# Optimization experiments

Hardware: AMD Instinct MI355X
Metric: run time of the kernel (lower is better)

Reference implementation:

```python
import jax, jax.numpy as jnp
import numpy as np

D = 1024
H = 16
HD = D // H
FF = 4096
B, S = 2, 2048


def _ln(x, g, b, eps):
    mu = jnp.mean(x, axis=-1, keepdims=True)
    var = jnp.mean(jnp.square(x - mu), axis=-1, keepdims=True)
    return (x - mu) * jax.lax.rsqrt(var + eps) * g + b


def setup_inputs() -> dict:
    key = jax.random.key(0)
    ks = jax.random.split(key, 12)
    s = 0.02
    return {
        "x": jax.random.normal(ks[0], (B, S, D), jnp.float32),
        "attention_mask": jnp.ones((B, 1, 1, S), jnp.int32),
        "wq": jax.random.normal(ks[1], (D, D), jnp.float32) * s,
        "bq": jnp.zeros((D,), jnp.float32),
        "wk": jax.random.normal(ks[2], (D, D), jnp.float32) * s,
        "bk": jnp.zeros((D,), jnp.float32),
        "wv": jax.random.normal(ks[3], (D, D), jnp.float32) * s,
        "bv": jnp.zeros((D,), jnp.float32),
        "wo": jax.random.normal(ks[4], (D, D), jnp.float32) * s,
        "bo": jnp.zeros((D,), jnp.float32),
        "ln1_g": jnp.ones((D,), jnp.float32),
        "ln1_b": jnp.zeros((D,), jnp.float32),
        "w1": jax.random.normal(ks[5], (D, FF), jnp.float32) * s,
        "b1": jnp.zeros((FF,), jnp.float32),
        "w2": jax.random.normal(ks[6], (FF, D), jnp.float32) * s,
        "b2": jnp.zeros((D,), jnp.float32),
        "lnf_g": jnp.ones((D,), jnp.float32),
        "lnf_b": jnp.zeros((D,), jnp.float32),
        "ln2_g": jnp.ones((D,), jnp.float32),
        "ln2_b": jnp.zeros((D,), jnp.float32),
    }


def reference(x, attention_mask, wq, bq, wk, bk, wv, bv, wo, bo,
              ln1_g, ln1_b, w1, b1, w2, b2, lnf_g, lnf_b, ln2_g, ln2_b):
    b, s, d = x.shape
    # --- naive multi-head self-attention ---
    q = (x @ wq + bq).reshape(b, s, H, HD).transpose(0, 2, 1, 3)  # [b,h,s,hd]
    k = (x @ wk + bk).reshape(b, s, H, HD).transpose(0, 2, 1, 3)
    v = (x @ wv + bv).reshape(b, s, H, HD).transpose(0, 2, 1, 3)
    scores = jnp.einsum('bhqd,bhkd->bhqk', q, k) / jnp.sqrt(jnp.float32(HD))
    scores = jnp.where(attention_mask == 0, jnp.float32(-1e9), scores)
    attn = jax.nn.softmax(scores, axis=-1)
    ctx = jnp.einsum('bhqk,bhkd->bhqd', attn, v)
    ctx = ctx.transpose(0, 2, 1, 3).reshape(b, s, d)
    attn_out = ctx @ wo + bo
    # residual + LayerNorm (eps=1e-5, torch default)
    x1 = _ln(x + attn_out, ln1_g, ln1_b, 1e-5)
    # --- BERT-style FFN with internal residual LN (eps=1e-12) ---
    h = jax.nn.gelu(x1 @ w1 + b1, approximate=False)
    ff = _ln(h @ w2 + b2 + x1, lnf_g, lnf_b, 1e-12)
    # --- outer residual + LayerNorm (eps=1e-5) ---
    return _ln(x1 + ff, ln2_g, ln2_b, 1e-5)
```

## Files before the change

### kernel.cpp

```cpp
#include <hip/hip_runtime.h>

#define DMODEL 1024
#define NHEAD  16
#define HDIM   64
#define FFDIM  4096
#define BATCH  2
#define SEQ    2048
#define MTOK   (BATCH*SEQ)

typedef __bf16 bf16;
typedef __bf16 bf16x8 __attribute__((ext_vector_type(8)));
typedef __bf16 bf16x4 __attribute__((ext_vector_type(4)));
typedef float  floatx4 __attribute__((ext_vector_type(4)));
typedef unsigned int u32;
typedef unsigned int u32x4 __attribute__((ext_vector_type(4)));

__device__ __forceinline__ int get_flag(const void* ln1g) {
  return (((const u32*)ln1g)[0] == 0x3F800000u) ? 0 : 1;
}
__device__ __forceinline__ float ld_ext(const void* p, size_t i, int flag) {
  return flag ? (float)((const bf16*)p)[i] : ((const float*)p)[i];
}

__device__ __forceinline__ void gload16(const bf16* g, bf16* lds_uniform) {
  __builtin_amdgcn_global_load_lds(
      (const __attribute__((address_space(1))) u32*)g,
      (__attribute__((address_space(3))) u32*)lds_uniform, 16, 0, 0);
}

__device__ __forceinline__ float gelu_f(float v) {
  float e = __expf(-1.702f * v);
  return __fdividef(v, 1.0f + e);
}

__global__ __launch_bounds__(256) void prep(
    const void* wq, const void* wk, const void* wv, const void* wo,
    const void* w1, const void* w2, const void* x, const int* mask,
    bf16* WTqkv, bf16* WToT, bf16* WT1, bf16* WT2, bf16* xC,
    u32* mwAll, bf16* m01All, const void* ln1g)
{
  int flag = get_flag(ln1g);
  int bid = blockIdx.x;
  if (bid >= 16384) {
    int b = bid - 16384;
    int base = b * SEQ + threadIdx.x * 8;
    #pragma unroll
    for (int j = 0; j < 8; j++)
      m01All[base + j] = (bf16)(mask[base + j] ? 1.0f : 0.0f);
    #pragma unroll
    for (int t = 0; t < 4; t++) {
      int k0 = threadIdx.x * 8 + 2 * t;
      u32 mw = (mask[b * SEQ + k0] ? 0x0000FFFFu : 0u) |
               (mask[b * SEQ + k0 + 1] ? 0xFFFF0000u : 0u);
      mwAll[b * (SEQ / 2) + threadIdx.x * 4 + t] = mw;
    }
    return;
  }
  if (bid >= 12288) {
    size_t base = (size_t)(bid - 12288) * 1024;
    int i = threadIdx.x * 4;
    #pragma unroll
    for (int j = 0; j < 4; j++) xC[base + i + j] = (bf16)ld_ext(x, base + i + j, flag);
    return;
  }
  __shared__ bf16 tile[32][33];
  const void* in; bf16* out; int K, N, t;
  if      (bid < 1024)  { in = wq; out = WTqkv;                 K = 1024; N = 1024; t = bid; }
  else if (bid < 2048)  { in = wk; out = WTqkv + 1024 * 1024;   K = 1024; N = 1024; t = bid - 1024; }
  else if (bid < 3072)  { in = wv; out = WTqkv + 2 * 1024 * 1024; K = 1024; N = 1024; t = bid - 2048; }
  else if (bid < 4096)  { in = wo; out = WToT;                  K = 1024; N = 1024; t = bid - 3072; }
  else if (bid < 8192)  { in = w1; out = WT1;                   K = 1024; N = 4096; t = bid - 4096; }
  else                  { in = w2; out = WT2;                   K = 4096; N = 1024; t = bid - 8192; }
  int shift = (N == 4096) ? 7 : 5;
  int k0 = (t >> shift) * 32, n0 = (t & ((1 << shift) - 1)) * 32;
  int tx = threadIdx.x & 31, ty = threadIdx.x >> 5;
  #pragma unroll
  for (int i = ty; i < 32; i += 8)
    tile[i][tx] = (bf16)ld_ext(in, (size_t)(k0 + i) * N + n0 + tx, flag);
  __syncthreads();
  #pragma unroll
  for (int i = ty; i < 32; i += 8)
    out[(size_t)(n0 + i) * K + k0 + tx] = tile[tx][i];
}

__global__ __launch_bounds__(256) void gemm128(
    const bf16* __restrict__ A, const bf16* __restrict__ BT,
    const void* __restrict__ bias0, const void* __restrict__ bias1,
    const void* __restrict__ bias2,
    bf16* __restrict__ out0, bf16* __restrict__ out1, bf16* __restrict__ out2,
    int N, int K, int ksub, int mode, const void* __restrict__ ln1g)
{
  __shared__ __align__(16) char smem[34816];
  bf16* As = (bf16*)smem;
  bf16* Bs = (bf16*)(smem + 16384);
  int flag = get_flag(ln1g);

  int tid = threadIdx.x, lane = tid & 63, w = tid >> 6;
  int wm = w & 1, wn = w >> 1;
  int m0 = blockIdx.x * 128, n0 = blockIdx.y * 128;
  int kstart = blockIdx.z * ksub;
  int r15 = lane & 15, kg = lane >> 4;

  floatx4 acc[4][4];
  #pragma unroll
  for (int mt = 0; mt < 4; mt++)
    #pragma unroll
    for (int nt = 0; nt < 4; nt++) acc[mt][nt] = (floatx4){0.f, 0.f, 0.f, 0.f};

  int srow8 = lane >> 3;
  int skc = (lane & 7) ^ (srow8 & 7);
  const bf16* Ap = A  + (size_t)(m0 + w * 32 + srow8) * K + kstart + skc * 8;
  const bf16* Bp = BT + (size_t)(n0 + w * 32 + srow8) * K + kstart + skc * 8;
  const size_t jstr = (size_t)8 * K;

  for (int it = ksub >> 6; it > 0; it--) {
    #pragma unroll
    for (int j = 0; j < 4; j++) {
      gload16(Ap + j * jstr, As + (size_t)(w * 256 + j * 64) * 8);
      gload16(Bp + j * jstr, Bs + (size_t)(w * 256 + j * 64) * 8);
    }
    Ap += 64; Bp += 64;
    __syncthreads();

    #pragma unroll
    for (int kk = 0; kk < 2; kk++) {
      bf16x8 af[4], bfr[4];
      #pragma unroll
      for (int mt = 0; mt < 4; mt++) {
        int row = wm * 64 + mt * 16 + r15;
        int slot = (kk * 4 + kg) ^ (r15 & 7);
        af[mt] = *(const bf16x8*)&As[(row * 8 + slot) * 8];
      }
      #pragma unroll
      for (int nt = 0; nt < 4; nt++) {
        int row = wn * 64 + nt * 16 + r15;
        int slot = (kk * 4 + kg) ^ (r15 & 7);
        bfr[nt] = *(const bf16x8*)&Bs[(row * 8 + slot) * 8];
      }
      #pragma unroll
      for (int mt = 0; mt < 4; mt++)
        #pragma unroll
        for (int nt = 0; nt < 4; nt++)
          acc[mt][nt] = __builtin_amdgcn_mfma_f32_16x16x32_bf16(af[mt], bfr[nt], acc[mt][nt], 0, 0, 0);
    }
    __syncthreads();
  }

  bf16* scr = (bf16*)(smem + 8704 * w);
  int gcb = n0 + wn * 64;
  int which = (mode == 1) ? (gcb >> 10) : 0;
  int rowg0 = m0 + wm * 64;

  #pragma unroll
  for (int nt = 0; nt < 4; nt++) {
    int lcol = nt * 16 + r15;
    int gcol = gcb + lcol;
    int bidx = (mode == 1) ? (gcol & 1023) : gcol;
    const void* bp = (mode == 1) ? ((which == 0) ? bias0 : (which == 1) ? bias1 : bias2) : bias0;
    float bv = (blockIdx.z == 0) ? ld_ext(bp, bidx, flag) : 0.f;
    #pragma unroll
    for (int mt = 0; mt < 4; mt++) {
      #pragma unroll
      for (int r = 0; r < 4; r++) {
        int lrow = mt * 16 + kg * 4 + r;
        float val = acc[mt][nt][r] + bv;
        if (mode == 2) val = gelu_f(val);
        if (mode == 1 && which == 0) val *= 0.125f;
        if (mode == 1 && which == 2) scr[lcol * 68 + lrow] = (bf16)val;
        else                         scr[lrow * 68 + lcol] = (bf16)val;
      }
    }
  }
  __syncthreads();

  bf16* outp = out0 + (size_t)blockIdx.z * MTOK * N;
  #pragma unroll
  for (int it = 0; it < 8; it++) {
    int c = it * 64 + lane;
    int rr = c >> 3, part = c & 7;
    bf16x8 vdat = *(const bf16x8*)&scr[rr * 68 + part * 8];
    bf16* dst;
    if (mode == 1) {
      if (which == 2) {
        int h = (gcb - 2048) >> 6, hd = rr;
        int b = rowg0 >> 11, s0 = rowg0 & 2047;
        dst = out2 + ((size_t)(b * NHEAD + h) * HDIM + hd) * SEQ + s0 + part * 8;
      } else {
        int rowg = rowg0 + rr;
        int b = rowg >> 11, s = rowg & 2047;
        int h = (gcb & 1023) >> 6;
        bf16* o = (which == 0) ? out0 : out1;
        dst = o + ((size_t)(b * NHEAD + h) * SEQ + s) * HDIM + part * 8;
      }
    } else {
      dst = outp + (size_t)(rowg0 + rr) * N + gcb + part * 8;
    }
    *(bf16x8*)dst = vdat;
  }
}

__global__ __launch_bounds__(256) void attn_mfma(
    const bf16* __restrict__ q, const bf16* __restrict__ k,
    const bf16* __restrict__ vt, const u32* __restrict__ mwAll,
    const bf16* __restrict__ m01All, bf16* __restrict__ ctx)
{
  __shared__ __align__(16) bf16 Ks[4096];
  __shared__ __align__(16) bf16 Vts[4096];
  __shared__ __align__(16) bf16 Ps[4][2048];

  int tid = threadIdx.x, lane = tid & 63, w = tid >> 6;
  int r15 = lane & 15, kg = lane >> 4;
  int x7 = r15 & 7;
  int bh = blockIdx.x >> 4;
  int qt = blockIdx.x & 15;
  int b = bh >> 4, h = bh & 15;
  int q0 = qt * 128 + w * 32;

  bf16x8 qf[2][2];
  #pragma unroll
  for (int mt = 0; mt < 2; mt++)
    #pragma unroll
    for (int kt2 = 0; kt2 < 2; kt2++)
      qf[mt][kt2] = *(const bf16x8*)(q + ((size_t)bh * SEQ + q0 + mt * 16 + r15) * HDIM + kt2 * 32 + kg * 8);

  floatx4 O[2][4];
  floatx4 lacc[2];
  #pragma unroll
  for (int mt = 0; mt < 2; mt++) {
    lacc[mt] = (floatx4){0.f, 0.f, 0.f, 0.f};
    #pragma unroll
    for (int dt = 0; dt < 4; dt++) O[mt][dt] = (floatx4){0.f, 0.f, 0.f, 0.f};
  }

  int slo = kg ^ x7, shi = (kg + 4) ^ x7;
  const bf16* pap[2][2];
  #pragma unroll
  for (int mt = 0; mt < 2; mt++) {
    pap[mt][0] = &Ps[w][((mt * 16 + r15) * 8 + slo) * 8];
    pap[mt][1] = &Ps[w][((mt * 16 + r15) * 8 + shi) * 8];
  }

  for (int kt = 0; kt < SEQ; kt += 64) {
    #pragma unroll
    for (int j = 0; j < 2; j++) {
      int c = w * 128 + j * 64 + lane;
      int row = c >> 3, cc = c & 7;
      gload16(k + ((size_t)bh * SEQ + kt + row) * HDIM + (cc ^ (row & 7)) * 8,
              Ks + (size_t)(w * 128 + j * 64) * 8);
    }
    #pragma unroll
    for (int j = 0; j < 2; j++) {
      int c = tid + j * 256;
      int row = c >> 3, cc = c & 7;
      u32x4 vv = *(const u32x4*)(vt + ((size_t)bh * HDIM + row) * SEQ + kt + cc * 8);
      u32x4 mw = *(const u32x4*)&mwAll[(size_t)b * (SEQ / 2) + (kt + cc * 8) / 2];
      vv &= mw;
      *(u32x4*)&Vts[(row * 8 + (cc ^ (row & 7))) * 8] = vv;
    }
    __syncthreads();

    floatx4 S[2][4];
    #pragma unroll
    for (int mt = 0; mt < 2; mt++)
      #pragma unroll
      for (int nt = 0; nt < 4; nt++) S[mt][nt] = (floatx4){0.f, 0.f, 0.f, 0.f};
    #pragma unroll
    for (int nt = 0; nt < 4; nt++) {
      int rb = (nt * 16 + r15) * 8;
      bf16x8 kf0 = *(const bf16x8*)&Ks[(rb + slo) * 8];
      bf16x8 kf1 = *(const bf16x8*)&Ks[(rb + shi) * 8];
      #pragma unroll
      for (int mt = 0; mt < 2; mt++) {
        S[mt][nt] = __builtin_amdgcn_mfma_f32_16x16x32_bf16(kf0, qf[mt][0], S[mt][nt], 0, 0, 0);
        S[mt][nt] = __builtin_amdgcn_mfma_f32_16x16x32_bf16(kf1, qf[mt][1], S[mt][nt], 0, 0, 0);
      }
    }

    #pragma unroll
    for (int mt = 0; mt < 2; mt++)
      #pragma unroll
      for (int nt = 0; nt < 4; nt++) {
        bf16x4 pk;
        #pragma unroll
        for (int r = 0; r < 4; r++) pk[r] = (bf16)__expf(S[mt][nt][r]);
        int c2 = 2 * nt + (kg >> 1);
        *(bf16x4*)&Ps[w][((mt * 16 + r15) * 8 + (c2 ^ x7)) * 8 + (kg & 1) * 4] = pk;
      }

    bf16x8 pa[2][2];
    #pragma unroll
    for (int mt = 0; mt < 2; mt++) {
      pa[mt][0] = *(const bf16x8*)pap[mt][0];
      pa[mt][1] = *(const bf16x8*)pap[mt][1];
    }
    bf16x8 m01f0 = *(const bf16x8*)&m01All[(size_t)b * SEQ + kt + kg * 8];
    bf16x8 m01f1 = *(const bf16x8*)&m01All[(size_t)b * SEQ + kt + 32 + kg * 8];
    #pragma unroll
    for (int dt = 0; dt < 4; dt++) {
      int rb = (dt * 16 + r15) * 8;
      bf16x8 vf0 = *(const bf16x8*)&Vts[(rb + slo) * 8];
      bf16x8 vf1 = *(const bf16x8*)&Vts[(rb + shi) * 8];
      #pragma unroll
      for (int mt = 0; mt < 2; mt++) {
        O[mt][dt] = __builtin_amdgcn_mfma_f32_16x16x32_bf16(pa[mt][0], vf0, O[mt][dt], 0, 0, 0);
        O[mt][dt] = __builtin_amdgcn_mfma_f32_16x16x32_bf16(pa[mt][1], vf1, O[mt][dt], 0, 0, 0);
      }
    }
    #pragma unroll
    for (int mt = 0; mt < 2; mt++) {
      lacc[mt] = __builtin_amdgcn_mfma_f32_16x16x32_bf16(pa[mt][0], m01f0, lacc[mt], 0, 0, 0);
      lacc[mt] = __builtin_amdgcn_mfma_f32_16x16x32_bf16(pa[mt][1], m01f1, lacc[mt], 0, 0, 0);
    }
    __syncthreads();
  }

  #pragma unroll
  for (int mt = 0; mt < 2; mt++) {
    float inv[4];
    #pragma unroll
    for (int r = 0; r < 4; r++) inv[r] = 1.f / lacc[mt][r];
    #pragma unroll
    for (int dt = 0; dt < 4; dt++)
      #pragma unroll
      for (int r = 0; r < 4; r++) {
        int srow = q0 + mt * 16 + kg * 4 + r;
        int col = h * 64 + dt * 16 + r15;
        ctx[((size_t)b * SEQ + srow) * DMODEL + col] = (bf16)(O[mt][dt][r] * inv[r]);
      }
  }
}

__global__ __launch_bounds__(256) void ln_kernel(
    const bf16* ba, const bf16* bb, const bf16* bc,
    const void* g, const void* be, float eps, bf16* outb, const void* ln1g)
{
  __shared__ float red1[4], red2[4];
  int flag = get_flag(ln1g);
  size_t base = (size_t)blockIdx.x * DMODEL;
  float v[4];
  #pragma unroll
  for (int i = 0; i < 4; i++) {
    int idx = threadIdx.x + i * 256;
    float s = (float)ba[base + idx] + (float)bb[base + idx] + (float)bc[base + idx];
    v[i] = s;
  }
  float sum = v[0] + v[1] + v[2] + v[3];
  #pragma unroll
  for (int o = 32; o > 0; o >>= 1) sum += __shfl_xor(sum, o);
  if ((threadIdx.x & 63) == 0) red1[threadIdx.x >> 6] = sum;
  __syncthreads();
  float mean = (red1[0] + red1[1] + red1[2] + red1[3]) * (1.f / DMODEL);
  float sq = 0.f;
  #pragma unroll
  for (int i = 0; i < 4; i++) { v[i] -= mean; sq += v[i] * v[i]; }
  #pragma unroll
  for (int o = 32; o > 0; o >>= 1) sq += __shfl_xor(sq, o);
  if ((threadIdx.x & 63) == 0) red2[threadIdx.x >> 6] = sq;
  __syncthreads();
  float rstd = rsqrtf((red2[0] + red2[1] + red2[2] + red2[3]) * (1.f / DMODEL) + eps);
  #pragma unroll
  for (int i = 0; i < 4; i++) {
    int idx = threadIdx.x + i * 256;
    outb[base + idx] = (bf16)(v[i] * rstd * ld_ext(g, idx, flag) + ld_ext(be, idx, flag));
  }
}

__global__ __launch_bounds__(256) void ln_double(
    const bf16* p0, const bf16* p1, const bf16* x1,
    const void* gf, const void* bf, const void* g2, const void* b2,
    void* out_ext, const void* ln1g)
{
  __shared__ float red1[4], red2[4];
  int flag = get_flag(ln1g);
  size_t base = (size_t)blockIdx.x * DMODEL;
  float xv[4], v[4];
  #pragma unroll
  for (int i = 0; i < 4; i++) {
    int idx = threadIdx.x + i * 256;
    xv[i] = (float)x1[base + idx];
    v[i] = xv[i] + (float)p0[base + idx] + (float)p1[base + idx];
  }
  float sum = v[0] + v[1] + v[2] + v[3];
  #pragma unroll
  for (int o = 32; o > 0; o >>= 1) sum += __shfl_xor(sum, o);
  if ((threadIdx.x & 63) == 0) red1[threadIdx.x >> 6] = sum;
  __syncthreads();
  float mean = (red1[0] + red1[1] + red1[2] + red1[3]) * (1.f / DMODEL);
  float sq = 0.f;
  #pragma unroll
  for (int i = 0; i < 4; i++) { v[i] -= mean; sq += v[i] * v[i]; }
  #pragma unroll
  for (int o = 32; o > 0; o >>= 1) sq += __shfl_xor(sq, o);
  if ((threadIdx.x & 63) == 0) red2[threadIdx.x >> 6] = sq;
  __syncthreads();
  float rstd = rsqrtf((red2[0] + red2[1] + red2[2] + red2[3]) * (1.f / DMODEL) + 1e-12f);
  #pragma unroll
  for (int i = 0; i < 4; i++) {
    int idx = threadIdx.x + i * 256;
    float ff = v[i] * rstd * ld_ext(gf, idx, flag) + ld_ext(bf, idx, flag);
    v[i] = xv[i] + (float)(bf16)ff;
  }
  __syncthreads();
  sum = v[0] + v[1] + v[2] + v[3];
  #pragma unroll
  for (int o = 32; o > 0; o >>= 1) sum += __shfl_xor(sum, o);
  if ((threadIdx.x & 63) == 0) red1[threadIdx.x >> 6] = sum;
  __syncthreads();
  mean = (red1[0] + red1[1] + red1[2] + red1[3]) * (1.f / DMODEL);
  sq = 0.f;
  #pragma unroll
  for (int i = 0; i < 4; i++) { v[i] -= mean; sq += v[i] * v[i]; }
  #pragma unroll
  for (int o = 32; o > 0; o >>= 1) sq += __shfl_xor(sq, o);
  if ((threadIdx.x & 63) == 0) red2[threadIdx.x >> 6] = sq;
  __syncthreads();
  rstd = rsqrtf((red2[0] + red2[1] + red2[2] + red2[3]) * (1.f / DMODEL) + 1e-5f);
  #pragma unroll
  for (int i = 0; i < 4; i++) {
    int idx = threadIdx.x + i * 256;
    float y = v[i] * rstd * ld_ext(g2, idx, flag) + ld_ext(b2, idx, flag);
    if (flag) ((bf16*)out_ext)[base + idx] = (bf16)y;
    else      ((float*)out_ext)[base + idx] = y;
  }
}

extern "C" void kernel_launch(void* const* d_in, const int* in_sizes, int n_in,
                              void* d_out, int out_size, void* d_ws, size_t ws_size,
                              hipStream_t stream) {
  const void* x    = d_in[0];
  const int*  msk  = (const int*)d_in[1];
  const void* wq   = d_in[2];
  const void* bq   = d_in[3];
  const void* wk   = d_in[4];
  const void* bk   = d_in[5];
  const void* wv   = d_in[6];
  const void* bv   = d_in[7];
  const void* wo   = d_in[8];
  const void* bo   = d_in[9];
  const void* ln1g = d_in[10];
  const void* ln1b = d_in[11];
  const void* w1   = d_in[12];
  const void* b1   = d_in[13];
  const void* w2   = d_in[14];
  const void* b2   = d_in[15];
  const void* lnfg = d_in[16];
  const void* lnfb = d_in[17];
  const void* ln2g = d_in[18];
  const void* ln2b = d_in[19];

  const size_t MB = 1024 * 1024;
  char* p = (char*)d_ws;
  bf16* xC     = (bf16*)(p + 0 * MB);
  bf16* qb     = (bf16*)(p + 8 * MB);
  bf16* kb     = (bf16*)(p + 16 * MB);
  bf16* vtb    = (bf16*)(p + 24 * MB);
  bf16* ctxb   = (bf16*)(p + 32 * MB);
  bf16* WTqkv  = (bf16*)(p + 40 * MB);
  bf16* WToT   = (bf16*)(p + 46 * MB);
  bf16* WT1    = (bf16*)(p + 48 * MB);
  bf16* WT2    = (bf16*)(p + 56 * MB);
  bf16* ao     = (bf16*)(p + 8 * MB);
  bf16* x1b    = xC;
  bf16* hb     = (bf16*)(p + 8 * MB);
  bf16* ffp    = (bf16*)(p + 40 * MB);
  u32*  mwAll  = (u32*)d_out;
  bf16* m01All = (bf16*)((char*)d_out + 8192);

  prep<<<16386, 256, 0, stream>>>(wq, wk, wv, wo, w1, w2, x, msk,
                                  WTqkv, WToT, WT1, WT2, xC, mwAll, m01All, ln1g);

  gemm128<<<dim3(MTOK / 128, 3072 / 128, 1), 256, 0, stream>>>(
      xC, WTqkv, bq, bk, bv, qb, kb, vtb, 3072, DMODEL, DMODEL, 1, ln1g);

  attn_mfma<<<BATCH * NHEAD * (SEQ / 128), 256, 0, stream>>>(qb, kb, vtb, mwAll, m01All, ctxb);

  gemm128<<<dim3(MTOK / 128, DMODEL / 128, 2), 256, 0, stream>>>(
      ctxb, WToT, bo, nullptr, nullptr, ao, nullptr, nullptr, DMODEL, DMODEL, 512, 3, ln1g);

  ln_kernel<<<MTOK, 256, 0, stream>>>(ao, ao + (size_t)MTOK * DMODEL, xC, ln1g, ln1b,
                                      1e-5f, x1b, ln1g);

  gemm128<<<dim3(MTOK / 128, FFDIM / 128, 1), 256, 0, stream>>>(
      x1b, WT1, b1, nullptr, nullptr, hb, nullptr, nullptr, FFDIM, DMODEL, DMODEL, 2, ln1g);

  gemm128<<<dim3(MTOK / 128, DMODEL / 128, 2), 256, 0, stream>>>(
      hb, WT2, b2, nullptr, nullptr, ffp, nullptr, nullptr, DMODEL, FFDIM, 2048, 3, ln1g);

  ln_double<<<MTOK, 256, 0, stream>>>(ffp, ffp + (size_t)MTOK * DMODEL, x1b,
                                      lnfg, lnfb, ln2g, ln2b, d_out, ln1g);
}
```

Baseline: 393.5 us.

## Halve GEMM K-step to 32 and split epilogue into two passes to cut LDS

The GEMM main loop now stages a 32-wide K slice per iteration instead of 64, with a new swizzled layout that packs two rows per 128-byte line. The epilogue writes the tile through shared memory in two half passes. Together these shrink shared memory from about 34 KB to 20 KB per block, so more blocks can be resident per CU. The cost is twice as many K iterations and barriers and extra synchronisation in the epilogue.

Result: slower. 412.0 us (+4.7%).

```diff
diff --git a/kernel.cpp b/kernel.cpp
--- a/kernel.cpp
+++ b/kernel.cpp
@@ -90,9 +90,9 @@
     bf16* __restrict__ out0, bf16* __restrict__ out1, bf16* __restrict__ out2,
     int N, int K, int ksub, int mode, const void* __restrict__ ln1g)
 {
-  __shared__ __align__(16) char smem[34816];
+  __shared__ __align__(16) char smem[20480];
   bf16* As = (bf16*)smem;
-  bf16* Bs = (bf16*)(smem + 16384);
+  bf16* Bs = (bf16*)(smem + 8192);
   int flag = get_flag(ln1g);
 
   int tid = threadIdx.x, lane = tid & 63, w = tid >> 6;
@@ -107,95 +107,110 @@
     #pragma unroll
     for (int nt = 0; nt < 4; nt++) acc[mt][nt] = (floatx4){0.f, 0.f, 0.f, 0.f};
 
-  int srow8 = lane >> 3;
-  int skc = (lane & 7) ^ (srow8 & 7);
-  const bf16* Ap = A  + (size_t)(m0 + w * 32 + srow8) * K + kstart + skc * 8;
-  const bf16* Bp = BT + (size_t)(n0 + w * 32 + srow8) * K + kstart + skc * 8;
-  const size_t jstr = (size_t)8 * K;
-
-  for (int it = ksub >> 6; it > 0; it--) {
-    #pragma unroll
-    for (int j = 0; j < 4; j++) {
-      gload16(Ap + j * jstr, As + (size_t)(w * 256 + j * 64) * 8);
-      gload16(Bp + j * jstr, Bs + (size_t)(w * 256 + j * 64) * 8);
-    }
-    Ap += 64; Bp += 64;
+  int c0 = w * 128 + lane;
+  int l0 = c0 >> 3;
+  int s2 = (c0 & 7) ^ (l0 & 7);
+  int srow = 2 * l0 + (s2 >> 2);
+  int skc = s2 & 3;
+  const bf16* Ap = A  + (size_t)(m0 + srow) * K + kstart + skc * 8;
+  const bf16* Bp = BT + (size_t)(n0 + srow) * K + kstart + skc * 8;
+  const size_t jstr = (size_t)16 * K;
+
+  int fslot = ((r15 & 1) * 4 + kg) ^ (r15 >> 1);
+
+  for (int it = ksub >> 5; it > 0; it--) {
+    #pragma unroll
+    for (int j = 0; j < 2; j++) {
+      gload16(Ap + j * jstr, As + (size_t)(w * 128 + j * 64) * 8);
+      gload16(Bp + j * jstr, Bs + (size_t)(w * 128 + j * 64) * 8);
+    }
+    Ap += 32; Bp += 32;
     __syncthreads();
 
-    #pragma unroll
-    for (int kk = 0; kk < 2; kk++) {
-      bf16x8 af[4], bfr[4];
-      #pragma unroll
-      for (int mt = 0; mt < 4; mt++) {
-        int row = wm * 64 + mt * 16 + r15;
-        int slot = (kk * 4 + kg) ^ (r15 & 7);
-        af[mt] = *(const bf16x8*)&As[(row * 8 + slot) * 8];
-      }
-      #pragma unroll
-      for (int nt = 0; nt < 4; nt++) {
-        int row = wn * 64 + nt * 16 + r15;
-        int slot = (kk * 4 + kg) ^ (r15 & 7);
-        bfr[nt] = *(const bf16x8*)&Bs[(row * 8 + slot) * 8];
-      }
-      #pragma unroll
-      for (int mt = 0; mt < 4; mt++)
-        #pragma unroll
-        for (int nt = 0; nt < 4; nt++)
-          acc[mt][nt] = __builtin_amdgcn_mfma_f32_16x16x32_bf16(af[mt], bfr[nt], acc[mt][nt], 0, 0, 0);
-    }
+    bf16x8 af[4], bfr[4];
+    #pragma unroll
+    for (int mt = 0; mt < 4; mt++) {
+      int line = wm * 32 + mt * 8 + (r15 >> 1);
+      af[mt] = *(const bf16x8*)&As[(line * 8 + fslot) * 8];
+    }
+    #pragma unroll
+    for (int nt = 0; nt < 4; nt++) {
+      int line = wn * 32 + nt * 8 + (r15 >> 1);
+      bfr[nt] = *(const bf16x8*)&Bs[(line * 8 + fslot) * 8];
+    }
+    #pragma unroll
+    for (int mt = 0; mt < 4; mt++)
+      #pragma unroll
+      for (int nt = 0; nt < 4; nt++)
+        acc[mt][nt] = __builtin_amdgcn_mfma_f32_16x16x32_bf16(af[mt], bfr[nt], acc[mt][nt], 0, 0, 0);
     __syncthreads();
   }
 
-  bf16* scr = (bf16*)(smem + 8704 * w);
+  bf16* scr = (bf16*)(smem + 5120 * w);
   int gcb = n0 + wn * 64;
   int which = (mode == 1) ? (gcb >> 10) : 0;
   int rowg0 = m0 + wm * 64;
-
+  bf16* outp = out0 + (size_t)blockIdx.z * MTOK * N;
+
+  float bvs[4];
   #pragma unroll
   for (int nt = 0; nt < 4; nt++) {
-    int lcol = nt * 16 + r15;
-    int gcol = gcb + lcol;
+    int gcol = gcb + nt * 16 + r15;
     int bidx = (mode == 1) ? (gcol & 1023) : gcol;
     const void* bp = (mode == 1) ? ((which == 0) ? bias0 : (which == 1) ? bias1 : bias2) : bias0;
-    float bv = (blockIdx.z == 0) ? ld_ext(bp, bidx, flag) : 0.f;
-    #pragma unroll
-    for (int mt = 0; mt < 4; mt++) {
-      #pragma unroll
-      for (int r = 0; r < 4; r++) {
-        int lrow = mt * 16 + kg * 4 + r;
-        float val = acc[mt][nt][r] + bv;
-        if (mode == 2) val = gelu_f(val);
-        if (mode == 1 && which == 0) val *= 0.125f;
-        if (mode == 1 && which == 2) scr[lcol * 68 + lrow] = (bf16)val;
-        else                         scr[lrow * 68 + lcol] = (bf16)val;
-      }
-    }
-  }
-  __syncthreads();
-
-  bf16* outp = out0 + (size_t)blockIdx.z * MTOK * N;
-  #pragma unroll
-  for (int it = 0; it < 8; it++) {
-    int c = it * 64 + lane;
-    int rr = c >> 3, part = c & 7;
-    bf16x8 vdat = *(const bf16x8*)&scr[rr * 68 + part * 8];
-    bf16* dst;
-    if (mode == 1) {
-      if (which == 2) {
-        int h = (gcb - 2048) >> 6, hd = rr;
-        int b = rowg0 >> 11, s0 = rowg0 & 2047;
-        dst = out2 + ((size_t)(b * NHEAD + h) * HDIM + hd) * SEQ + s0 + part * 8;
-      } else {
-        int rowg = rowg0 + rr;
-        int b = rowg >> 11, s = rowg & 2047;
-        int h = (gcb & 1023) >> 6;
-        bf16* o = (which == 0) ? out0 : out1;
-        dst = o + ((size_t)(b * NHEAD + h) * SEQ + s) * HDIM + part * 8;
+    bvs[nt] = (blockIdx.z == 0) ? ld_ext(bp, bidx, flag) : 0.f;
+  }
+
+  #pragma unroll
+  for (int pass = 0; pass < 2; pass++) {
+    __syncthreads();
+    #pragma unroll
+    for (int mh = 0; mh < 2; mh++) {
+      int mt = 2 * pass + mh;
+      #pragma unroll
+      for (int nt = 0; nt < 4; nt++) {
+        int lcol = nt * 16 + r15;
+        #pragma unroll
+        for (int r = 0; r < 4; r++) {
+          int lrow = mh * 16 + kg * 4 + r;
+          float val = acc[mt][nt][r] + bvs[nt];
+          if (mode == 2) val = gelu_f(val);
+          if (mode == 1 && which == 0) val *= 0.125f;
+          if (mode == 1 && which == 2) scr[lcol * 40 + lrow] = (bf16)val;
+          else                         scr[lrow * 68 + lcol] = (bf16)val;
+        }
+      }
+    }
+    __syncthreads();
+    if (mode == 1 && which == 2) {
+      int hh = (gcb - 2048) >> 6;
+      int b = rowg0 >> 11, s0 = rowg0 & 2047;
+      #pragma unroll
+      for (int it = 0; it < 4; it++) {
+        int c = it * 64 + lane;
+        int cc = c >> 2, part = c & 3;
+        bf16x8 vdat = *(const bf16x8*)&scr[cc * 40 + part * 8];
+        *(bf16x8*)(out2 + ((size_t)(b * NHEAD + hh) * HDIM + cc) * SEQ + s0 + pass * 32 + part * 8) = vdat;
       }
     } else {
-      dst = outp + (size_t)(rowg0 + rr) * N + gcb + part * 8;
-    }
-    *(bf16x8*)dst = vdat;
+      #pragma unroll
+      for (int it = 0; it < 4; it++) {
+        int c = it * 64 + lane;
+        int rr = c >> 3, part = c & 7;
+        bf16x8 vdat = *(const bf16x8*)&scr[rr * 68 + part * 8];
+        int rowg = rowg0 + pass * 32 + rr;
+        bf16* dst;
+        if (mode == 1) {
+          int b = rowg >> 11, s = rowg & 2047;
+          int hh = (gcb & 1023) >> 6;
+          bf16* o = (which == 0) ? out0 : out1;
+          dst = o + ((size_t)(b * NHEAD + hh) * SEQ + s) * HDIM + part * 8;
+        } else {
+          dst = outp + (size_t)rowg * N + gcb + part * 8;
+        }
+        *(bf16x8*)dst = vdat;
+      }
+    }
   }
 }
 
@@ -341,8 +356,7 @@
   #pragma unroll
   for (int i = 0; i < 4; i++) {
     int idx = threadIdx.x + i * 256;
-    float s = (float)ba[base + idx] + (float)bb[base + idx] + (float)bc[base + idx];
-    v[i] = s;
+    v[i] = (float)ba[base + idx] + (float)bb[base + idx] + (float)bc[base + idx];
   }
   float sum = v[0] + v[1] + v[2] + v[3];
   #pragma unroll
```
